# Performance work log

Hardware: AMD Instinct MI355X
Metric: run time of the kernel (lower is better)

## Reference

```python
import jax, jax.numpy as jnp
import numpy as np
from jax import lax

B, C_IN, C_OUT, T, D = 8, 32, 32, 2048, 32
L = T + 1  # max_timesteps=2048 is even -> pos length 2049


def setup_inputs() -> dict:
    key = jax.random.key(0)
    ks = jax.random.split(key, 8)
    x = jax.random.normal(ks[0], (B, C_IN, T), dtype=jnp.float32)
    # register_buffer pos_rel = linspace(-1, 1, L) with shape (1, 1, L)
    pos_rel = jnp.linspace(-1.0, 1.0, L, dtype=jnp.float32).reshape(1, 1, L)
    # SIREN init: first Conv1d weight ~ U(-1,1); later layers ~ U(-val,val), val=sqrt(6/in)/omega_0 (omega_0=1)
    w1 = jax.random.uniform(ks[1], (D, 1), jnp.float32, -1.0, 1.0)
    b1 = jax.random.uniform(ks[2], (D,), jnp.float32, -1.0, 1.0)
    val2 = float(np.sqrt(6.0 / D))
    w2 = jax.random.uniform(ks[3], (D, D), jnp.float32, -val2, val2)
    b2 = jax.random.uniform(ks[4], (D,), jnp.float32, -val2, val2)
    w3 = jax.random.uniform(ks[5], (C_OUT * C_IN, D), jnp.float32, -val2, val2)
    b3 = jax.random.uniform(ks[6], (C_OUT * C_IN,), jnp.float32, -val2, val2)
    bias = jax.random.normal(ks[7], (C_OUT,), dtype=jnp.float32)
    return {"x": x, "pos_rel": pos_rel, "w1": w1, "b1": b1, "w2": w2,
            "b2": b2, "w3": w3, "b3": b3, "bias": bias}


def reference(x, pos_rel, w1, b1, w2, b2, w3, b3, bias):
    # Kernel network (all kernel_size-1 convs == pointwise matmuls over positions).
    # Note: Sine.forward is sin(linear(x)); omega_0 param is unused in forward.
    p = pos_rel[0]                                   # (1, L)
    h = jnp.sin(w1 @ p + b1[:, None])                # (D, L)
    h = jnp.sin(w2 @ h + b2[:, None])                # (D, L)
    k = w3 @ h + b3[:, None]                         # (C_OUT*C_IN, L)
    kernel = k.reshape(C_OUT, C_IN, L)               # conv weight (O, I, K)
    # Causal left-padding with K-1 zeros, then VALID cross-correlation (torch conv1d semantics).
    xp = jnp.pad(x, ((0, 0), (0, 0), (L - 1, 0)))    # (B, C_IN, T+L-1)
    out = lax.conv_general_dilated(xp, kernel, window_strides=(1,), padding='VALID',
                                   dimension_numbers=('NCH', 'OIH', 'NCH'))
    return out + bias[None, :, None]                 # (B, C_OUT, T)
```

## Files before the change

### kernel.cpp

```cpp
#include <hip/hip_runtime.h>
#include <hip/hip_bf16.h>

#define BATCH 8
#define TLEN 2048
#define PADR 256
#define XT_ROWS (TLEN + PADR + 64)
#define GT_BYTES (2048*1024*2)
#define XT_BYTES (BATCH*XT_ROWS*32*2)
#define PART_OFF ((GT_BYTES + XT_BYTES + 255) & ~255)
#define JOBS_PER_B 144
#define NJOBS (BATCH*JOBS_PER_B)

using short8 = __attribute__((ext_vector_type(8))) short;
using f32x4  = __attribute__((ext_vector_type(4))) float;

__global__ void gen_kernel(const float* __restrict__ pos, const float* __restrict__ w1,
                           const float* __restrict__ b1, const float* __restrict__ w2,
                           const float* __restrict__ b2, const float* __restrict__ w3,
                           const float* __restrict__ b3, __hip_bfloat16* __restrict__ Gt) {
    __shared__ float t1s[8][33];
    __shared__ float h2s[8][33];
    int tid = threadIdx.x;
    int d0 = blockIdx.x * 8;
    int dl = tid >> 5, jj = tid & 31;
    {
        int d = d0 + dl;
        float p = pos[2048 - d];
        t1s[dl][jj] = sinf(w1[jj] * p + b1[jj]);
    }
    __syncthreads();
    {
        float a = b2[jj];
        #pragma unroll
        for (int k = 0; k < 32; ++k) a += w2[jj*32 + k] * t1s[dl][k];
        h2s[dl][jj] = sinf(a);
    }
    __syncthreads();
    for (int r = 0; r < 32; ++r) {
        int idx = r*256 + tid;
        int dl2 = idx >> 10, oi = idx & 1023;
        float a = b3[oi];
        #pragma unroll
        for (int k = 0; k < 32; ++k) a += w3[oi*32 + k] * h2s[dl2][k];
        Gt[(size_t)(d0 + dl2)*1024 + oi] = __float2bfloat16(a);
    }
}

__global__ void transpose_x(const float* __restrict__ x, __hip_bfloat16* __restrict__ xT) {
    __shared__ float tile[32][65];
    int tid = threadIdx.x;
    int b = blockIdx.x >> 5;
    int c = blockIdx.x & 31;
    int t0 = c * 64;
    #pragma unroll
    for (int r = 0; r < 8; ++r) {
        int i  = r*4 + (tid >> 6);
        int tl = tid & 63;
        tile[i][tl] = x[((size_t)(b*32 + i))*TLEN + t0 + tl];
    }
    __syncthreads();
    #pragma unroll
    for (int r = 0; r < 8; ++r) {
        int idx = r*256 + tid;
        int tl = idx >> 5, i = idx & 31;
        xT[((size_t)(b*XT_ROWS + PADR + t0 + tl))*32 + i] = __float2bfloat16(tile[i][tl]);
    }
    if (c == 0) {
        for (int idx = tid; idx < PADR*32; idx += 256)
            xT[(size_t)b*XT_ROWS*32 + idx] = __float2bfloat16(0.0f);
    }
    if (c == 1) {
        for (int idx = tid; idx < 64*32; idx += 256)
            xT[((size_t)b*XT_ROWS + PADR + TLEN)*32 + idx] = __float2bfloat16(0.0f);
    }
}

#define MFMA8(A0,A1,A2,A3,B0,B1)                                                  \
    acc[0][0] = __builtin_amdgcn_mfma_f32_16x16x32_bf16(A0, B0, acc[0][0], 0,0,0); \
    acc[0][1] = __builtin_amdgcn_mfma_f32_16x16x32_bf16(A0, B1, acc[0][1], 0,0,0); \
    acc[1][0] = __builtin_amdgcn_mfma_f32_16x16x32_bf16(A1, B0, acc[1][0], 0,0,0); \
    acc[1][1] = __builtin_amdgcn_mfma_f32_16x16x32_bf16(A1, B1, acc[1][1], 0,0,0); \
    acc[2][0] = __builtin_amdgcn_mfma_f32_16x16x32_bf16(A2, B0, acc[2][0], 0,0,0); \
    acc[2][1] = __builtin_amdgcn_mfma_f32_16x16x32_bf16(A2, B1, acc[2][1], 0,0,0); \
    acc[3][0] = __builtin_amdgcn_mfma_f32_16x16x32_bf16(A3, B0, acc[3][0], 0,0,0); \
    acc[3][1] = __builtin_amdgcn_mfma_f32_16x16x32_bf16(A3, B1, acc[3][1], 0,0,0);

#define LDA  a0 = lds_a[ab]; a1 = lds_a[ab+80]; a2 = lds_a[ab+160]; a3 = lds_a[ab+240]; ab -= 5;

__global__ __launch_bounds__(256) void conv_mfma(const __hip_bfloat16* __restrict__ GtB,
                                                 const __hip_bfloat16* __restrict__ xTB,
                                                 float* __restrict__ partial) {
    __shared__ short8 lds_a[320*5];
    int tid  = threadIdx.x;
    int lane = tid & 63;
    int w    = tid >> 6;
    int jid  = blockIdx.x;
    int b    = jid / JOBS_PER_B;
    int r    = jid - b * JOBS_PER_B;
    int J = (int)((sqrtf(2.0f*r + 1.0f) - 1.0f) * 0.5f);
    while (2*(J+1)*(J+2) <= r) ++J;
    while (2*J*(J+1) > r) --J;
    int S  = r - 2*J*(J+1);
    int d0 = 64*S;

    const short8* xs = (const short8*)xTB;
    int g0 = b*XT_ROWS + PADR + 256*J - 64*S - 63;
    #pragma unroll
    for (int c = 0; c < 5; ++c) {
        int lr = c*64 + (tid >> 2);
        lds_a[lr*5 + (tid & 3)] = xs[(size_t)(g0 + lr)*4 + (tid & 3)];
    }
    __syncthreads();

    int l15 = lane & 15, l4 = lane >> 4;
    const short8* gp = (const short8*)GtB + (size_t)d0*128 + l15*4 + l4;
    int ab = (63 + 64*w + l15)*5 + l4;

    f32x4 acc[4][2];
    const f32x4 zero = {0.f, 0.f, 0.f, 0.f};
    #pragma unroll
    for (int mt = 0; mt < 4; ++mt) { acc[mt][0] = zero; acc[mt][1] = zero; }

    short8 bx0 = gp[0], bx1 = gp[64]; gp += 128;
    short8 by0, by1, a0, a1, a2, a3;

    for (int it = 0; it < 31; ++it) {
        by0 = gp[0]; by1 = gp[64]; gp += 128;
        LDA MFMA8(a0, a1, a2, a3, bx0, bx1)
        bx0 = gp[0]; bx1 = gp[64]; gp += 128;
        LDA MFMA8(a0, a1, a2, a3, by0, by1)
    }
    by0 = gp[0]; by1 = gp[64];
    LDA MFMA8(a0, a1, a2, a3, bx0, bx1)
    LDA MFMA8(a0, a1, a2, a3, by0, by1)

    float* pw = partial + (size_t)jid * 8192;
    #pragma unroll
    for (int no = 0; no < 2; ++no)
        #pragma unroll
        for (int mt = 0; mt < 4; ++mt) {
            int addr = (16*no + l15)*256 + 64*w + 16*mt + l4*4;
            *reinterpret_cast<f32x4*>(pw + addr) = acc[mt][no];
        }
}

__global__ void reduce_out(const float* __restrict__ partial, const float* __restrict__ bias,
                           float* __restrict__ out) {
    int gid = blockIdx.x * 256 + threadIdx.x;
    int tl = gid & 255;
    int J  = (gid >> 8) & 7;
    int o  = (gid >> 11) & 31;
    int b  = gid >> 16;
    int jid = b*JOBS_PER_B + 2*J*(J+1);
    int cnt = 4*(J+1);
    const float* p = partial + (size_t)jid*8192 + o*256 + tl;
    float s0 = 0.f, s1 = 0.f, s2 = 0.f, s3 = 0.f;
    for (int sg = 0; sg < cnt; sg += 4) {
        s0 += p[(size_t)sg*8192];
        s1 += p[(size_t)(sg+1)*8192];
        s2 += p[(size_t)(sg+2)*8192];
        s3 += p[(size_t)(sg+3)*8192];
    }
    out[((size_t)(b*32 + o))*TLEN + 256*J + tl] = bias[o] + ((s0 + s1) + (s2 + s3));
}

extern "C" void kernel_launch(void* const* d_in, const int* in_sizes, int n_in,
                              void* d_out, int out_size, void* d_ws, size_t ws_size,
                              hipStream_t stream) {
    const float* x    = (const float*)d_in[0];
    const float* pos  = (const float*)d_in[1];
    const float* w1   = (const float*)d_in[2];
    const float* b1   = (const float*)d_in[3];
    const float* w2   = (const float*)d_in[4];
    const float* b2   = (const float*)d_in[5];
    const float* w3   = (const float*)d_in[6];
    const float* b3   = (const float*)d_in[7];
    const float* bias = (const float*)d_in[8];
    float* out = (float*)d_out;

    char* ws = (char*)d_ws;
    __hip_bfloat16* Gt = (__hip_bfloat16*)ws;
    __hip_bfloat16* xT = (__hip_bfloat16*)(ws + GT_BYTES);
    float* partial     = (float*)(ws + PART_OFF);

    hipLaunchKernelGGL(gen_kernel,  dim3(256),   dim3(256), 0, stream,
                       pos, w1, b1, w2, b2, w3, b3, Gt);
    hipLaunchKernelGGL(transpose_x, dim3(256),   dim3(256), 0, stream, x, xT);
    hipLaunchKernelGGL(conv_mfma,   dim3(NJOBS), dim3(256), 0, stream, Gt, xT, partial);
    hipLaunchKernelGGL(reduce_out,  dim3(2048),  dim3(256), 0, stream, partial, bias, out);
}
```

Measured before the change: 163.6 us.

## Fuse prep kernels, swizzle LDS, and stream half the A operands from global

Merges the kernel-generation and x-transpose kernels into a single launch, with block index selecting the role, to save a launch and let both run concurrently. The MLP dot products are split into two partial accumulators for more ILP. In the conv kernel the LDS tile uses an XOR-swizzled 4-slot layout instead of 5-slot padding to avoid bank conflicts. Only two of the four A fragments per step come from LDS; the other two are loaded straight from global memory with software prefetch, trading LDS traffic for more global or cache loads.

```diff
diff --git a/kernel.cpp b/kernel.cpp
--- a/kernel.cpp
+++ b/kernel.cpp
@@ -14,64 +14,70 @@
 using short8 = __attribute__((ext_vector_type(8))) short;
 using f32x4  = __attribute__((ext_vector_type(4))) float;
 
-__global__ void gen_kernel(const float* __restrict__ pos, const float* __restrict__ w1,
-                           const float* __restrict__ b1, const float* __restrict__ w2,
-                           const float* __restrict__ b2, const float* __restrict__ w3,
-                           const float* __restrict__ b3, __hip_bfloat16* __restrict__ Gt) {
-    __shared__ float t1s[8][33];
-    __shared__ float h2s[8][33];
+__global__ void prep_kernel(const float* __restrict__ pos, const float* __restrict__ w1,
+                            const float* __restrict__ b1, const float* __restrict__ w2,
+                            const float* __restrict__ b2, const float* __restrict__ w3,
+                            const float* __restrict__ b3, const float* __restrict__ x,
+                            __hip_bfloat16* __restrict__ Gt, __hip_bfloat16* __restrict__ xT) {
+    __shared__ float smem[32][65];
     int tid = threadIdx.x;
-    int d0 = blockIdx.x * 8;
-    int dl = tid >> 5, jj = tid & 31;
-    {
-        int d = d0 + dl;
-        float p = pos[2048 - d];
-        t1s[dl][jj] = sinf(w1[jj] * p + b1[jj]);
-    }
-    __syncthreads();
-    {
-        float a = b2[jj];
+    if (blockIdx.x < 256) {
+        float* t1s = &smem[0][0];
+        float* h2s = &smem[8][0];
+        int d0 = blockIdx.x * 8;
+        int dl = tid >> 5, jj = tid & 31;
+        {
+            float p = pos[2048 - (d0 + dl)];
+            t1s[dl*33 + jj] = sinf(w1[jj] * p + b1[jj]);
+        }
+        __syncthreads();
+        {
+            float s0 = 0.f, s1 = 0.f;
+            #pragma unroll
+            for (int k = 0; k < 16; ++k) {
+                s0 += w2[jj*32 + k]      * t1s[dl*33 + k];
+                s1 += w2[jj*32 + 16 + k] * t1s[dl*33 + 16 + k];
+            }
+            h2s[dl*33 + jj] = sinf(b2[jj] + s0 + s1);
+        }
+        __syncthreads();
+        for (int r = 0; r < 32; ++r) {
+            int idx = r*256 + tid;
+            int dl2 = idx >> 10, oi = idx & 1023;
+            float s0 = 0.f, s1 = 0.f;
+            #pragma unroll
+            for (int k = 0; k < 16; ++k) {
+                s0 += w3[oi*32 + k]      * h2s[dl2*33 + k];
+                s1 += w3[oi*32 + 16 + k] * h2s[dl2*33 + 16 + k];
+            }
+            Gt[(size_t)(d0 + dl2)*1024 + oi] = __float2bfloat16(b3[oi] + s0 + s1);
+        }
+    } else {
+        int blk = blockIdx.x - 256;
+        int b = blk >> 5;
+        int c = blk & 31;
+        int t0 = c * 64;
         #pragma unroll
-        for (int k = 0; k < 32; ++k) a += w2[jj*32 + k] * t1s[dl][k];
-        h2s[dl][jj] = sinf(a);
-    }
-    __syncthreads();
-    for (int r = 0; r < 32; ++r) {
-        int idx = r*256 + tid;
-        int dl2 = idx >> 10, oi = idx & 1023;
-        float a = b3[oi];
+        for (int r = 0; r < 8; ++r) {
+            int i  = r*4 + (tid >> 6);
+            int tl = tid & 63;
+            smem[i][tl] = x[((size_t)(b*32 + i))*TLEN + t0 + tl];
+        }
+        __syncthreads();
         #pragma unroll
-        for (int k = 0; k < 32; ++k) a += w3[oi*32 + k] * h2s[dl2][k];
-        Gt[(size_t)(d0 + dl2)*1024 + oi] = __float2bfloat16(a);
-    }
-}
-
-__global__ void transpose_x(const float* __restrict__ x, __hip_bfloat16* __restrict__ xT) {
-    __shared__ float tile[32][65];
-    int tid = threadIdx.x;
-    int b = blockIdx.x >> 5;
-    int c = blockIdx.x & 31;
-    int t0 = c * 64;
-    #pragma unroll
-    for (int r = 0; r < 8; ++r) {
-        int i  = r*4 + (tid >> 6);
-        int tl = tid & 63;
-        tile[i][tl] = x[((size_t)(b*32 + i))*TLEN + t0 + tl];
-    }
-    __syncthreads();
-    #pragma unroll
-    for (int r = 0; r < 8; ++r) {
-        int idx = r*256 + tid;
-        int tl = idx >> 5, i = idx & 31;
-        xT[((size_t)(b*XT_ROWS + PADR + t0 + tl))*32 + i] = __float2bfloat16(tile[i][tl]);
-    }
-    if (c == 0) {
-        for (int idx = tid; idx < PADR*32; idx += 256)
-            xT[(size_t)b*XT_ROWS*32 + idx] = __float2bfloat16(0.0f);
-    }
-    if (c == 1) {
-        for (int idx = tid; idx < 64*32; idx += 256)
-            xT[((size_t)b*XT_ROWS + PADR + TLEN)*32 + idx] = __float2bfloat16(0.0f);
+        for (int r = 0; r < 8; ++r) {
+            int idx = r*256 + tid;
+            int tl = idx >> 5, i = idx & 31;
+            xT[((size_t)(b*XT_ROWS + PADR + t0 + tl))*32 + i] = __float2bfloat16(smem[i][tl]);
+        }
+        if (c == 0) {
+            for (int idx = tid; idx < PADR*32; idx += 256)
+                xT[(size_t)b*XT_ROWS*32 + idx] = __float2bfloat16(0.0f);
+        }
+        if (c == 1) {
+            for (int idx = tid; idx < 64*32; idx += 256)
+                xT[((size_t)b*XT_ROWS + PADR + TLEN)*32 + idx] = __float2bfloat16(0.0f);
+        }
     }
 }
 
@@ -85,12 +91,12 @@
     acc[3][0] = __builtin_amdgcn_mfma_f32_16x16x32_bf16(A3, B0, acc[3][0], 0,0,0); \
     acc[3][1] = __builtin_amdgcn_mfma_f32_16x16x32_bf16(A3, B1, acc[3][1], 0,0,0);
 
-#define LDA  a0 = lds_a[ab]; a1 = lds_a[ab+80]; a2 = lds_a[ab+160]; a3 = lds_a[ab+240]; ab -= 5;
+#define LDA2 { int ai = r0*4 + (l4 ^ ((r0 >> 1) & 3)); a0 = lds_a[ai]; a1 = lds_a[ai + 64]; r0--; }
 
 __global__ __launch_bounds__(256) void conv_mfma(const __hip_bfloat16* __restrict__ GtB,
                                                  const __hip_bfloat16* __restrict__ xTB,
                                                  float* __restrict__ partial) {
-    __shared__ short8 lds_a[320*5];
+    __shared__ short8 lds_a[320*4];
     int tid  = threadIdx.x;
     int lane = tid & 63;
     int w    = tid >> 6;
@@ -107,14 +113,16 @@
     int g0 = b*XT_ROWS + PADR + 256*J - 64*S - 63;
     #pragma unroll
     for (int c = 0; c < 5; ++c) {
-        int lr = c*64 + (tid >> 2);
-        lds_a[lr*5 + (tid & 3)] = xs[(size_t)(g0 + lr)*4 + (tid & 3)];
+        int lr   = c*64 + (tid >> 2);
+        int slot = tid & 3;
+        lds_a[lr*4 + (slot ^ ((lr >> 1) & 3))] = xs[(size_t)(g0 + lr)*4 + slot];
     }
     __syncthreads();
 
     int l15 = lane & 15, l4 = lane >> 4;
-    const short8* gp = (const short8*)GtB + (size_t)d0*128 + l15*4 + l4;
-    int ab = (63 + 64*w + l15)*5 + l4;
+    const short8* gp  = (const short8*)GtB + (size_t)d0*128 + l15*4 + l4;
+    const short8* gap = xs + (size_t)(g0 + 95 + 64*w + l15)*4 + l4;
+    int r0 = 63 + 64*w + l15;
 
     f32x4 acc[4][2];
     const f32x4 zero = {0.f, 0.f, 0.f, 0.f};
@@ -122,17 +130,25 @@
     for (int mt = 0; mt < 4; ++mt) { acc[mt][0] = zero; acc[mt][1] = zero; }
 
     short8 bx0 = gp[0], bx1 = gp[64]; gp += 128;
-    short8 by0, by1, a0, a1, a2, a3;
+    short8 gx2 = gap[0], gx3 = gap[64]; gap -= 4;
+    short8 by0, by1, gy2, gy3, a0, a1;
 
     for (int it = 0; it < 31; ++it) {
         by0 = gp[0]; by1 = gp[64]; gp += 128;
-        LDA MFMA8(a0, a1, a2, a3, bx0, bx1)
+        gy2 = gap[0]; gy3 = gap[64]; gap -= 4;
+        LDA2
+        MFMA8(a0, a1, gx2, gx3, bx0, bx1)
         bx0 = gp[0]; bx1 = gp[64]; gp += 128;
-        LDA MFMA8(a0, a1, a2, a3, by0, by1)
+        gx2 = gap[0]; gx3 = gap[64]; gap -= 4;
+        LDA2
+        MFMA8(a0, a1, gy2, gy3, by0, by1)
     }
     by0 = gp[0]; by1 = gp[64];
-    LDA MFMA8(a0, a1, a2, a3, bx0, bx1)
-    LDA MFMA8(a0, a1, a2, a3, by0, by1)
+    gy2 = gap[0]; gy3 = gap[64];
+    LDA2
+    MFMA8(a0, a1, gx2, gx3, bx0, bx1)
+    LDA2
+    MFMA8(a0, a1, gy2, gy3, by0, by1)
 
     float* pw = partial + (size_t)jid * 8192;
     #pragma unroll
@@ -183,9 +199,8 @@
     __hip_bfloat16* xT = (__hip_bfloat16*)(ws + GT_BYTES);
     float* partial     = (float*)(ws + PART_OFF);
 
-    hipLaunchKernelGGL(gen_kernel,  dim3(256),   dim3(256), 0, stream,
-                       pos, w1, b1, w2, b2, w3, b3, Gt);
-    hipLaunchKernelGGL(transpose_x, dim3(256),   dim3(256), 0, stream, x, xT);
+    hipLaunchKernelGGL(prep_kernel, dim3(512),   dim3(256), 0, stream,
+                       pos, w1, b1, w2, b2, w3, b3, x, Gt, xT);
     hipLaunchKernelGGL(conv_mfma,   dim3(NJOBS), dim3(256), 0, stream, Gt, xT, partial);
     hipLaunchKernelGGL(reduce_out,  dim3(2048),  dim3(256), 0, stream, partial, bias, out);
 }
```

Result: slower. 197.0 us (+20.4%).
